# Optimization experiments

Hardware: AMD Instinct MI355X
Metric: run time of the kernel (lower is better)

The kernel has to match this reference:

```python
import jax, jax.numpy as jnp
import numpy as np

K_PERIODS = 4   # k_periods
PMAX = 64       # pmax
MIN_P = 16      # min_period_threshold (already clamped to <= PMAX)


def setup_inputs() -> dict:
    key = jax.random.key(0)
    B, T, N = 32, 512, 128
    x = jax.random.normal(key, (B, T, N), dtype=jnp.float32)
    return {"x": x}


def reference(x):
    # x: [B, T, N]
    B, T, N = x.shape
    K = K_PERIODS
    seqs = jnp.transpose(x, (0, 2, 1)).reshape(B * N, T)  # [BN, T]

    # top-k nonzero frequencies by rFFT amplitude
    spec = jnp.fft.rfft(seqs, axis=-1)                    # [BN, T//2+1]
    amp = jnp.abs(spec)
    amp = amp.at[..., 0].set(0.0)                         # zero DC component
    kamp, kidx = jax.lax.top_k(amp, K)                    # [BN, K] each
    kidx = jnp.maximum(kidx, 1)

    # periods and cycle counts
    P = jnp.clip(T // kidx, MIN_P, PMAX)                  # [BN, K]
    cycles = jnp.maximum(T // P, 1)                       # [BN, K]
    take = cycles * P

    # static upper bound on cycles (torch uses data-dependent cycles.max();
    # extra trailing cycle slots here are fully masked to zero)
    Cmax = T // MIN_P
    idx_c = jnp.arange(Cmax)                              # [Cmax]
    idx_p = jnp.arange(PMAX)                              # [Pmax]

    base = jnp.maximum(T - take, 0)[..., None, None]      # [BN, K, 1, 1]
    indices = base + idx_c[None, None, :, None] * P[..., None, None] \
              + idx_p[None, None, None, :]                # [BN, K, Cmax, Pmax]
    indices = jnp.clip(indices, 0, T - 1)

    # gather: broadcast seqs over (K, Cmax)
    gathered = jnp.take_along_axis(seqs[:, None, None, :], indices, axis=-1)

    mask = ((idx_c[None, None, :, None] < cycles[..., None, None]) &
            (idx_p[None, None, None, :] < P[..., None, None])).astype(x.dtype)
    gathered = gathered * mask

    gathered = gathered.reshape(B, N, K, Cmax, PMAX)
    mask = mask.reshape(B, N, K, Cmax, PMAX)
    kamp = kamp.reshape(B, N, K)
    return gathered, mask, kamp
```

## Files before the change

kernel.cpp:

```cpp
#include <hip/hip_runtime.h>
#include <math.h>

#define TLEN 512
#define NCH  128
#define KP   4
#define PMAXV 64
#define CMAXV 32
#define MINP 16
#define NSEQ 4096
#define OUTG ((size_t)NSEQ * KP * CMAXV * PMAXV)

#define PAD8(i) ((i) + ((i) >> 3))
#define ZP   290
#define SEQP 520

typedef float nfloat4 __attribute__((ext_vector_type(4)));

__global__ __launch_bounds__(256) void periodicity_kernel(
    const float* __restrict__ x,
    float* __restrict__ out_g,
    float* __restrict__ out_m,
    float* __restrict__ out_a)
{
    const int tid  = threadIdx.x;
    const int lane = tid & 63;
    const int w    = tid >> 6;
    const int s0   = blockIdx.x << 2;
    const int b    = s0 >> 7;
    const int n0   = s0 & (NCH - 1);

    __shared__ float   seqf[4 * SEQP];
    __shared__ double2 Z[4 * ZP];
    __shared__ double2 W[256];

    {
        const int col = tid & 3;
        const int t0  = tid >> 2;
        const float* base = x + (size_t)b * TLEN * NCH + n0 + col;
        #pragma unroll
        for (int it = 0; it < 8; ++it) {
            const int t = t0 + 64 * it;
            seqf[col * SEQP + t] = base[(size_t)t * NCH];
        }
        double ang = -6.283185307179586476925286766559 * (double)tid / (double)TLEN;
        double sv, cv;
        sincos(ang, &sv, &cv);
        W[tid] = make_double2(cv, sv);
    }
    __syncthreads();

    float*   sf = seqf + w * SEQP;
    double2* Zw = Z + w * ZP;

    #pragma unroll
    for (int u = 0; u < 4; ++u) {
        const int i = lane + 64 * u;
        const int r = (int)(__brev((unsigned)i) >> 24);
        const float2 p = ((const float2*)sf)[r];
        Zw[PAD8(i)] = make_double2((double)p.x, (double)p.y);
    }
    __builtin_amdgcn_wave_barrier();

    for (int st = 1; st <= 8; ++st) {
        const int half = 1 << (st - 1);
        #pragma unroll
        for (int u = 0; u < 2; ++u) {
            const int j   = lane + 64 * u;
            const int pos = j & (half - 1);
            const int i1  = ((j >> (st - 1)) << st) + pos;
            const int i2  = i1 + half;
            const double2 wv = W[pos << (9 - st)];
            const double2 a  = Zw[PAD8(i1)];
            const double2 c  = Zw[PAD8(i2)];
            const double tr = wv.x * c.x - wv.y * c.y;
            const double ti = wv.x * c.y + wv.y * c.x;
            Zw[PAD8(i1)] = make_double2(a.x + tr, a.y + ti);
            Zw[PAD8(i2)] = make_double2(a.x - tr, a.y - ti);
        }
        __builtin_amdgcn_wave_barrier();
    }

    double av[5];
    int    bins[5];
    #pragma unroll
    for (int u = 0; u < 4; ++u) {
        const int k = lane + 64 * u;
        const double2 zk = Zw[PAD8(k)];
        const double2 zm = Zw[PAD8((256 - k) & 255)];
        const double gr = 0.5 * (zk.x + zm.x);
        const double gi = 0.5 * (zk.y - zm.y);
        const double hr = 0.5 * (zk.y + zm.y);
        const double hi = 0.5 * (zm.x - zk.x);
        const double2 wv = W[k];
        const double xr = gr + wv.x * hr - wv.y * hi;
        const double xi = gi + wv.x * hi + wv.y * hr;
        av[u]   = (k == 0) ? 0.0 : (xr * xr + xi * xi);
        bins[u] = k;
    }
    av[4]   = -1.0;
    bins[4] = 256;
    if (lane == 0) {
        const double2 z0 = Zw[PAD8(0)];
        const double nyq = z0.x - z0.y;
        av[4] = nyq * nyq;
    }

    double bv[KP];
    int    bi[KP];
    #pragma unroll
    for (int q = 0; q < KP; ++q) {
        double v  = av[0];
        int    vi = bins[0];
        #pragma unroll
        for (int j = 1; j < 5; ++j)
            if (av[j] > v) { v = av[j]; vi = bins[j]; }
        #pragma unroll
        for (int off = 32; off > 0; off >>= 1) {
            const double ov = __shfl_xor(v, off, 64);
            const int    oi = __shfl_xor(vi, off, 64);
            if (ov > v || (ov == v && oi < vi)) { v = ov; vi = oi; }
        }
        bv[q] = v; bi[q] = vi;
        #pragma unroll
        for (int j = 0; j < 5; ++j)
            if (bins[j] == vi) av[j] = -1.0;
    }

    const int s = s0 + w;
    if (lane < KP) {
        double v = lane == 0 ? bv[0] : lane == 1 ? bv[1] : lane == 2 ? bv[2] : bv[3];
        out_a[(size_t)s * KP + lane] = (float)sqrt(v);
    }

    float* og = out_g + (size_t)s * (KP * CMAXV * PMAXV);
    float* om = out_m + (size_t)s * (KP * CMAXV * PMAXV);
    const int pp   = (lane & 15) << 2;
    const int crow = lane >> 4;

    #pragma unroll
    for (int k = 0; k < KP; ++k) {
        int ki = bi[k] < 1 ? 1 : bi[k];
        int P  = TLEN / ki;
        P = P < MINP ? MINP : (P > PMAXV ? PMAXV : P);
        const int cyc  = TLEN / P;
        const int base = TLEN - cyc * P;

        nfloat4 mrow;
        mrow.x = (pp     < P) ? 1.f : 0.f;
        mrow.y = (pp + 1 < P) ? 1.f : 0.f;
        mrow.z = (pp + 2 < P) ? 1.f : 0.f;
        mrow.w = (pp + 3 < P) ? 1.f : 0.f;

        float* ogk = og + k * (CMAXV * PMAXV) + pp;
        float* omk = om + k * (CMAXV * PMAXV) + pp;

        #pragma unroll
        for (int c8 = 0; c8 < 8; ++c8) {
            const int c = crow + 4 * c8;
            const bool live = c < cyc;
            nfloat4 m = (nfloat4)(0.f, 0.f, 0.f, 0.f);
            nfloat4 g = (nfloat4)(0.f, 0.f, 0.f, 0.f);
            if (live) {
                m = mrow;
                const int idx = base + c * P + pp;
                if (pp     < P) g.x = sf[idx];
                if (pp + 1 < P) g.y = sf[idx + 1];
                if (pp + 2 < P) g.z = sf[idx + 2];
                if (pp + 3 < P) g.w = sf[idx + 3];
            }
            *(nfloat4*)(omk + c * PMAXV) = m;
            *(nfloat4*)(ogk + c * PMAXV) = g;
        }
    }
}

extern "C" void kernel_launch(void* const* d_in, const int* in_sizes, int n_in,
                              void* d_out, int out_size, void* d_ws, size_t ws_size,
                              hipStream_t stream) {
    const float* x = (const float*)d_in[0];
    float* out = (float*)d_out;
    float* og = out;
    float* om = out + OUTG;
    float* oa = om + OUTG;

    periodicity_kernel<<<dim3(NSEQ / 4), dim3(256), 0, stream>>>(x, og, om, oa);
}
```

Measured before the change: 266.8 us.

## Split FFT/top-k and gather/store into separate kernels with nontemporal stores

```diff
diff --git a/kernel.cpp b/kernel.cpp
--- a/kernel.cpp
+++ b/kernel.cpp
@@ -16,11 +16,11 @@
 
 typedef float nfloat4 __attribute__((ext_vector_type(4)));
 
-__global__ __launch_bounds__(256) void periodicity_kernel(
+
+__global__ __launch_bounds__(256) void fft_topk_kernel(
     const float* __restrict__ x,
-    float* __restrict__ out_g,
-    float* __restrict__ out_m,
-    float* __restrict__ out_a)
+    float* __restrict__ out_a,
+    int4* __restrict__ bins)
 {
     const int tid  = threadIdx.x;
     const int lane = tid & 63;
@@ -81,7 +81,7 @@
     }
 
     double av[5];
-    int    bins[5];
+    int    binv[5];
     #pragma unroll
     for (int u = 0; u < 4; ++u) {
         const int k = lane + 64 * u;
@@ -95,10 +95,10 @@
         const double xr = gr + wv.x * hr - wv.y * hi;
         const double xi = gi + wv.x * hi + wv.y * hr;
         av[u]   = (k == 0) ? 0.0 : (xr * xr + xi * xi);
-        bins[u] = k;
+        binv[u] = k;
     }
     av[4]   = -1.0;
-    bins[4] = 256;
+    binv[4] = 256;
     if (lane == 0) {
         const double2 z0 = Zw[PAD8(0)];
         const double nyq = z0.x - z0.y;
@@ -110,10 +110,10 @@
     #pragma unroll
     for (int q = 0; q < KP; ++q) {
         double v  = av[0];
-        int    vi = bins[0];
+        int    vi = binv[0];
         #pragma unroll
         for (int j = 1; j < 5; ++j)
-            if (av[j] > v) { v = av[j]; vi = bins[j]; }
+            if (av[j] > v) { v = av[j]; vi = binv[j]; }
         #pragma unroll
         for (int off = 32; off > 0; off >>= 1) {
             const double ov = __shfl_xor(v, off, 64);
@@ -123,7 +123,7 @@
         bv[q] = v; bi[q] = vi;
         #pragma unroll
         for (int j = 0; j < 5; ++j)
-            if (bins[j] == vi) av[j] = -1.0;
+            if (binv[j] == vi) av[j] = -1.0;
     }
 
     const int s = s0 + w;
@@ -131,19 +131,53 @@
         double v = lane == 0 ? bv[0] : lane == 1 ? bv[1] : lane == 2 ? bv[2] : bv[3];
         out_a[(size_t)s * KP + lane] = (float)sqrt(v);
     }
+    if (lane == 0)
+        bins[s] = make_int4(bi[0], bi[1], bi[2], bi[3]);
+}
+
+__global__ __launch_bounds__(512, 8) void gather_store_kernel(
+    const float* __restrict__ x,
+    const int4* __restrict__ bins,
+    float* __restrict__ out_g,
+    float* __restrict__ out_m)
+{
+    const int tid  = threadIdx.x;
+    const int lane = tid & 63;
+    const int w    = tid >> 6;
+    const int s0   = blockIdx.x << 2;
+    const int b    = s0 >> 7;
+    const int n0   = s0 & (NCH - 1);
+
+    __shared__ float seqf[4 * SEQP];
+
+    const int col = tid & 3;
+    const int t0  = tid >> 2;
+    const float* xb = x + (size_t)b * TLEN * NCH + n0 + col;
+    const float stage0 = xb[(size_t)(t0      ) * NCH];
+    const float stage1 = xb[(size_t)(t0 + 128) * NCH];
+    const float stage2 = xb[(size_t)(t0 + 256) * NCH];
+    const float stage3 = xb[(size_t)(t0 + 384) * NCH];
+
+    const int ls = w >> 1;
+    const int kb = (w & 1) << 1;
+    const int s  = s0 + ls;
+    const int4 bn = bins[s];
+
+    const int pp   = (lane & 15) << 2;
+    const int crow = lane >> 4;
 
     float* og = out_g + (size_t)s * (KP * CMAXV * PMAXV);
     float* om = out_m + (size_t)s * (KP * CMAXV * PMAXV);
-    const int pp   = (lane & 15) << 2;
-    const int crow = lane >> 4;
-
-    #pragma unroll
-    for (int k = 0; k < KP; ++k) {
-        int ki = bi[k] < 1 ? 1 : bi[k];
-        int P  = TLEN / ki;
+    const nfloat4 zero = (nfloat4)(0.f, 0.f, 0.f, 0.f);
+
+    #pragma unroll
+    for (int kk = 0; kk < 2; ++kk) {
+        const int k = kb + kk;
+        int ki = (k == 0) ? bn.x : (k == 1) ? bn.y : (k == 2) ? bn.z : bn.w;
+        if (ki < 1) ki = 1;
+        int P = TLEN / ki;
         P = P < MINP ? MINP : (P > PMAXV ? PMAXV : P);
-        const int cyc  = TLEN / P;
-        const int base = TLEN - cyc * P;
+        const int cyc = TLEN / P;
 
         nfloat4 mrow;
         mrow.x = (pp     < P) ? 1.f : 0.f;
@@ -151,25 +185,49 @@
         mrow.z = (pp + 2 < P) ? 1.f : 0.f;
         mrow.w = (pp + 3 < P) ? 1.f : 0.f;
 
-        float* ogk = og + k * (CMAXV * PMAXV) + pp;
         float* omk = om + k * (CMAXV * PMAXV) + pp;
-
         #pragma unroll
         for (int c8 = 0; c8 < 8; ++c8) {
             const int c = crow + 4 * c8;
-            const bool live = c < cyc;
-            nfloat4 m = (nfloat4)(0.f, 0.f, 0.f, 0.f);
-            nfloat4 g = (nfloat4)(0.f, 0.f, 0.f, 0.f);
-            if (live) {
-                m = mrow;
+            __builtin_nontemporal_store(c < cyc ? mrow : zero,
+                                        (nfloat4*)(omk + c * PMAXV));
+        }
+    }
+
+    {
+        float* sc = seqf + col * SEQP;
+        sc[t0      ] = stage0;
+        sc[t0 + 128] = stage1;
+        sc[t0 + 256] = stage2;
+        sc[t0 + 384] = stage3;
+    }
+    __syncthreads();
+
+    const float* sf = seqf + ls * SEQP;
+
+    #pragma unroll
+    for (int kk = 0; kk < 2; ++kk) {
+        const int k = kb + kk;
+        int ki = (k == 0) ? bn.x : (k == 1) ? bn.y : (k == 2) ? bn.z : bn.w;
+        if (ki < 1) ki = 1;
+        int P = TLEN / ki;
+        P = P < MINP ? MINP : (P > PMAXV ? PMAXV : P);
+        const int cyc  = TLEN / P;
+        const int base = TLEN - cyc * P;
+
+        float* ogk = og + k * (CMAXV * PMAXV) + pp;
+        #pragma unroll
+        for (int c8 = 0; c8 < 8; ++c8) {
+            const int c = crow + 4 * c8;
+            nfloat4 g = zero;
+            if (c < cyc) {
                 const int idx = base + c * P + pp;
                 if (pp     < P) g.x = sf[idx];
                 if (pp + 1 < P) g.y = sf[idx + 1];
                 if (pp + 2 < P) g.z = sf[idx + 2];
                 if (pp + 3 < P) g.w = sf[idx + 3];
             }
-            *(nfloat4*)(omk + c * PMAXV) = m;
-            *(nfloat4*)(ogk + c * PMAXV) = g;
+            __builtin_nontemporal_store(g, (nfloat4*)(ogk + c * PMAXV));
         }
     }
 }
@@ -182,6 +240,8 @@
     float* og = out;
     float* om = out + OUTG;
     float* oa = om + OUTG;
-
-    periodicity_kernel<<<dim3(NSEQ / 4), dim3(256), 0, stream>>>(x, og, om, oa);
+    int4*  bins = (int4*)d_ws;
+
+    fft_topk_kernel<<<dim3(NSEQ / 4), dim3(256), 0, stream>>>(x, oa, bins);
+    gather_store_kernel<<<dim3(NSEQ / 4), dim3(512), 0, stream>>>(x, bins, og, om);
 }
```

New measurement: 285.9 us. 1.07x slower.

## Replace radix-2 FFT stages with radix-4 butterflies in LDS

Applied to the files above, without the earlier changes.

```diff
diff --git a/kernel.cpp b/kernel.cpp
--- a/kernel.cpp
+++ b/kernel.cpp
@@ -31,7 +31,7 @@
 
     __shared__ float   seqf[4 * SEQP];
     __shared__ double2 Z[4 * ZP];
-    __shared__ double2 W[256];
+    __shared__ double2 W[384];
 
     {
         const int col = tid & 3;
@@ -46,6 +46,8 @@
         double sv, cv;
         sincos(ang, &sv, &cv);
         W[tid] = make_double2(cv, sv);
+        if (tid < 128)
+            W[256 + tid] = make_double2(-cv, -sv);
     }
     __syncthreads();
 
@@ -55,28 +57,49 @@
     #pragma unroll
     for (int u = 0; u < 4; ++u) {
         const int i = lane + 64 * u;
-        const int r = (int)(__brev((unsigned)i) >> 24);
+        const int rb = (int)(__brev((unsigned)i) >> 24);
+        const int r  = ((rb >> 1) & 0x55) | ((rb & 0x55) << 1);
         const float2 p = ((const float2*)sf)[r];
         Zw[PAD8(i)] = make_double2((double)p.x, (double)p.y);
     }
     __builtin_amdgcn_wave_barrier();
 
-    for (int st = 1; st <= 8; ++st) {
-        const int half = 1 << (st - 1);
-        #pragma unroll
-        for (int u = 0; u < 2; ++u) {
-            const int j   = lane + 64 * u;
-            const int pos = j & (half - 1);
-            const int i1  = ((j >> (st - 1)) << st) + pos;
-            const int i2  = i1 + half;
-            const double2 wv = W[pos << (9 - st)];
-            const double2 a  = Zw[PAD8(i1)];
-            const double2 c  = Zw[PAD8(i2)];
-            const double tr = wv.x * c.x - wv.y * c.y;
-            const double ti = wv.x * c.y + wv.y * c.x;
-            Zw[PAD8(i1)] = make_double2(a.x + tr, a.y + ti);
-            Zw[PAD8(i2)] = make_double2(a.x - tr, a.y - ti);
-        }
+    #pragma unroll
+    for (int s4 = 0; s4 < 4; ++s4) {
+        const int Q = 1 << (2 * s4);
+        const int j = lane & (Q - 1);
+        const int o = ((lane >> (2 * s4)) << (2 * s4 + 2)) + j;
+
+        double2 A  = Zw[PAD8(o)];
+        double2 Bv = Zw[PAD8(o + Q)];
+        double2 Cv = Zw[PAD8(o + 2 * Q)];
+        double2 Dv = Zw[PAD8(o + 3 * Q)];
+
+        if (s4 > 0) {
+            const int t = j * (128 >> (2 * s4));
+            const double2 w1 = W[t];
+            const double2 w2 = W[2 * t];
+            const double2 w3 = W[3 * t];
+            double br = Bv.x * w1.x - Bv.y * w1.y;
+            double bi = Bv.x * w1.y + Bv.y * w1.x;
+            Bv = make_double2(br, bi);
+            double cr = Cv.x * w2.x - Cv.y * w2.y;
+            double ci = Cv.x * w2.y + Cv.y * w2.x;
+            Cv = make_double2(cr, ci);
+            double dr = Dv.x * w3.x - Dv.y * w3.y;
+            double di = Dv.x * w3.y + Dv.y * w3.x;
+            Dv = make_double2(dr, di);
+        }
+
+        const double t0r = A.x + Cv.x, t0i = A.y + Cv.y;
+        const double t1r = A.x - Cv.x, t1i = A.y - Cv.y;
+        const double t2r = Bv.x + Dv.x, t2i = Bv.y + Dv.y;
+        const double t3r = Bv.x - Dv.x, t3i = Bv.y - Dv.y;
+
+        Zw[PAD8(o)]         = make_double2(t0r + t2r, t0i + t2i);
+        Zw[PAD8(o + Q)]     = make_double2(t1r + t3i, t1i - t3r);
+        Zw[PAD8(o + 2 * Q)] = make_double2(t0r - t2r, t0i - t2i);
+        Zw[PAD8(o + 3 * Q)] = make_double2(t1r - t3i, t1i + t3r);
         __builtin_amdgcn_wave_barrier();
     }
 
```

Measured after the change: 264.9 us (median of 2 runs). No clear change (-0.7%).
